# Kernel optimization log

Measured on AMD Instinct MI355X. Metric: run time of the kernel, lower is better.

Reference implementation:

```python
import jax, jax.numpy as jnp
import numpy as np

B, L = 32, 4096
OBS_DIM, ACT_DIM = 32, 8
D_MODEL, D_STATE, N_LAYERS = 64, 16, 2
EXPAND, D_CONV = 2, 4
D_INNER = EXPAND * D_MODEL          # 128
DT_RANK = -(-D_MODEL // 16)         # ceil(64/16) = 4


def _layer_norm(x, w, b, eps=1e-5):
    m = x.mean(-1, keepdims=True)
    v = ((x - m) ** 2).mean(-1, keepdims=True)
    return (x - m) * jax.lax.rsqrt(v + eps) * w + b


def _mamba_block(x, in_proj_W, conv_w, conv_b, x_proj_W, dt_proj_W, dt_proj_b, A_log, D, out_proj_W):
    # x: (B, L, d_model) -> (B, L, d_model)
    xz = jnp.einsum('bld,ed->ble', x, in_proj_W)              # (B, L, 2*d_inner)
    u, z = jnp.split(xz, 2, axis=-1)
    # causal depthwise conv over time (groups = d_inner)
    uc = jax.lax.conv_general_dilated(u.swapaxes(1, 2), conv_w, (1,), [(D_CONV - 1, 0)],
                                      feature_group_count=D_INNER)
    u = jax.nn.silu((uc + conv_b[None, :, None]).swapaxes(1, 2))  # (B, L, d_inner)
    proj = jnp.einsum('bld,ed->ble', u, x_proj_W)             # (B, L, dt_rank + 2*d_state)
    dt = jax.nn.softplus(jnp.einsum('blr,dr->bld', proj[..., :DT_RANK], dt_proj_W) + dt_proj_b)
    Bm = proj[..., DT_RANK:DT_RANK + D_STATE]                 # (B, L, d_state)
    Cm = proj[..., DT_RANK + D_STATE:]                        # (B, L, d_state)
    A = -jnp.exp(A_log)                                       # (d_inner, d_state)

    def step(h, inp):
        u_t, dt_t, B_t, C_t = inp                              # (B,d_inner),(B,d_inner),(B,d_state),(B,d_state)
        h = h * jnp.exp(dt_t[..., None] * A) + (dt_t * u_t)[..., None] * B_t[:, None, :]
        return h, jnp.einsum('bds,bs->bd', h, C_t)

    h0 = jnp.zeros((x.shape[0], D_INNER, D_STATE), x.dtype)
    _, ys = jax.lax.scan(step, h0, (u.swapaxes(0, 1), dt.swapaxes(0, 1),
                                    Bm.swapaxes(0, 1), Cm.swapaxes(0, 1)))
    y = ys.swapaxes(0, 1) + u * D                              # skip term D*u
    y = y * jax.nn.silu(z)                                     # gated output
    return jnp.einsum('bld,od->blo', y, out_proj_W)


def setup_inputs() -> dict:
    key = jax.random.key(0)
    ks = jax.random.split(key, 10)
    s = 0.05
    return {
        'obs': jax.random.normal(ks[0], (B, L, OBS_DIM), jnp.float32),
        'obs_mean': jnp.zeros((OBS_DIM,), jnp.float32),
        'obs_scale': jnp.ones((OBS_DIM,), jnp.float32),
        'ln_in_w': jnp.ones((OBS_DIM,), jnp.float32),
        'ln_in_b': jnp.zeros((OBS_DIM,), jnp.float32),
        'W_in': jax.random.normal(ks[1], (D_MODEL, OBS_DIM), jnp.float32) * s,
        'b_in': jnp.zeros((D_MODEL,), jnp.float32),
        'norm_w': jnp.ones((N_LAYERS, D_MODEL), jnp.float32),
        'norm_b': jnp.zeros((N_LAYERS, D_MODEL), jnp.float32),
        'in_proj_W': jax.random.normal(ks[2], (N_LAYERS, 2 * D_INNER, D_MODEL), jnp.float32) * s,
        'conv_w': jax.random.normal(ks[3], (N_LAYERS, D_INNER, 1, D_CONV), jnp.float32) * s,
        'conv_b': jnp.zeros((N_LAYERS, D_INNER), jnp.float32),
        'x_proj_W': jax.random.normal(ks[4], (N_LAYERS, DT_RANK + 2 * D_STATE, D_INNER), jnp.float32) * s,
        'dt_proj_W': jax.random.normal(ks[5], (N_LAYERS, D_INNER, DT_RANK), jnp.float32) * s,
        'dt_proj_b': jax.random.normal(ks[6], (N_LAYERS, D_INNER), jnp.float32) * s,
        'A_log': jnp.log(jnp.broadcast_to(jnp.arange(1, D_STATE + 1, dtype=jnp.float32), (N_LAYERS, D_INNER, D_STATE))),
        'D': jnp.ones((N_LAYERS, D_INNER), jnp.float32),
        'out_proj_W': jax.random.normal(ks[7], (N_LAYERS, D_MODEL, D_INNER), jnp.float32) * s,
        'W_out': jax.random.normal(ks[8], (ACT_DIM, D_MODEL), jnp.float32) * s,
        'b_out': jnp.zeros((ACT_DIM,), jnp.float32),
    }


def reference(obs, obs_mean, obs_scale, ln_in_w, ln_in_b, W_in, b_in, norm_w, norm_b,
              in_proj_W, conv_w, conv_b, x_proj_W, dt_proj_W, dt_proj_b, A_log, D,
              out_proj_W, W_out, b_out):
    x = (obs - obs_mean) / obs_scale                 # _normalize_observations
    x = _layer_norm(x, ln_in_w, ln_in_b)             # input_norm
    x = jnp.einsum('blo,do->bld', x, W_in) + b_in    # input_layer
    for i in range(N_LAYERS):                        # x = x + block(norm(x))
        x = x + _mamba_block(_layer_norm(x, norm_w[i], norm_b[i]),
                             in_proj_W[i], conv_w[i], conv_b[i], x_proj_W[i],
                             dt_proj_W[i], dt_proj_b[i], A_log[i], D[i], out_proj_W[i])
    return jnp.einsum('bld,ad->bla', x, W_out) + b_out  # output_layer
```

## Files before the change

kernel.cpp:

```cpp
#include <hip/hip_runtime.h>
#include <hip/hip_bf16.h>

#define BB 32
#define LL 4096
#define DI 128
#define DSS 16
#define NLAY 2
#define NC 128
#define CT 32
#define MROWS (BB*LL)

typedef short v8s __attribute__((ext_vector_type(8)));
typedef float v4f __attribute__((ext_vector_type(4)));
#define MFMA16(a,b,c) __builtin_amdgcn_mfma_f32_16x16x32_bf16(a,b,c,0,0,0)

#define B_X     0ull
#define B_UCOOK 16777216ull
#define B_Z     50331648ull
#define B_DTY   83886080ull
#define B_BC    117440512ull
#define B_H     125829120ull
#define B_SDT   142606336ull
#define B_WGT   144703488ull
#define B_PACK  144977920ull

#define WM_OMEAN   0
#define WM_OSCALE  32
#define WM_LNW     64
#define WM_LNB     96
#define WM_WIN     128
#define WM_BIN     2176
#define WM_NORMW   2240
#define WM_NORMB   2368
#define WM_INPROJ  2496
#define WM_CONVW   35264
#define WM_CONVB   36288
#define WM_XPROJ   36544
#define WM_DTW     45760
#define WM_DTB     46784
#define WM_ALOG    47040
#define WM_D       51136
#define WM_OUTPROJ 51392
#define WM_WOUT    67776
#define WM_BOUT    68288

#define PK_WIN 0
#define PK_INP 2048
#define PK_XP  34816
#define PK_OP  47104

__device__ __forceinline__ float ldf(const void* p, long long i, bool bf) {
  if (bf) {
    unsigned int u = ((unsigned int)((const unsigned short*)p)[i]) << 16;
    float f; __builtin_memcpy(&f, &u, 4); return f;
  }
  return ((const float*)p)[i];
}
__device__ __forceinline__ float s2f(short s){
  unsigned int u = ((unsigned int)(unsigned short)s) << 16;
  float f; __builtin_memcpy(&f, &u, 4); return f;
}
__device__ __forceinline__ short f2s(float f){
  unsigned int u; __builtin_memcpy(&u, &f, 4);
  u += 0x7fffu + ((u >> 16) & 1u);
  return (short)(u >> 16);
}
__device__ __forceinline__ float siluf(float x){
  return x * __builtin_amdgcn_rcpf(1.f + __expf(-x));
}
__device__ __forceinline__ float softplusf(float x){
  return fmaxf(x,0.f) + __logf(1.f + __expf(-fabsf(x)));
}
__device__ __forceinline__ void powtree(float e1, float pw[16]){
  pw[0]=e1; pw[1]=e1*e1; pw[3]=pw[1]*pw[1]; pw[7]=pw[3]*pw[3]; pw[15]=pw[7]*pw[7];
  pw[2]=pw[1]*e1; pw[4]=pw[3]*e1; pw[5]=pw[3]*pw[1]; pw[6]=pw[3]*pw[2];
  pw[8]=pw[7]*e1; pw[9]=pw[7]*pw[1]; pw[10]=pw[7]*pw[2]; pw[11]=pw[7]*pw[3];
  pw[12]=pw[7]*pw[4]; pw[13]=pw[7]*pw[5]; pw[14]=pw[7]*pw[6];
}

struct PtrPack { const void* p[19]; };

__global__ __launch_bounds__(256) void k_cvt(PtrPack pp, float* __restrict__ dst,
                                             short* __restrict__ pk) {
  bool bf = ((const unsigned short*)pp.p[14])[1] != 0;
  int b = blockIdx.x;
  if (b < 19) {
    const int SZ[19] = {32,32,32,32,2048,64,128,128,32768,1024,256,9216,1024,256,4096,256,16384,512,8};
    const int OF[19] = {WM_OMEAN,WM_OSCALE,WM_LNW,WM_LNB,WM_WIN,WM_BIN,WM_NORMW,WM_NORMB,
                        WM_INPROJ,WM_CONVW,WM_CONVB,WM_XPROJ,WM_DTW,WM_DTB,WM_ALOG,WM_D,
                        WM_OUTPROJ,WM_WOUT,WM_BOUT};
    const void* src = pp.p[b];
    int n = SZ[b], o = OF[b];
    for (int j = threadIdx.x; j < n; j += 256) dst[o + j] = ldf(src, j, bf);
  } else {
    int pi = b - 19;
    const int SRC[7]  = {4,8,8,11,11,16,16};
    const int LOFF[7] = {0,0,16384,0,4608,0,8192};
    const int NTA[7]  = {4,16,16,3,3,4,4};
    const int KTA[7]  = {1,2,2,4,4,4,4};
    const int KA[7]   = {32,64,64,128,128,128,128};
    const int NRA[7]  = {64,256,256,36,36,64,64};
    const int DOFF[7] = {PK_WIN, PK_INP, PK_INP+16384, PK_XP, PK_XP+6144, PK_OP, PK_OP+8192};
    const void* src = pp.p[SRC[pi]];
    int ktc = KTA[pi], K = KA[pi], nr = NRA[pi], doff = DOFF[pi], loff = LOFF[pi];
    int tot = NTA[pi]*ktc*512;
    for (int i = threadIdx.x; i < tot; i += 256) {
      int j = i & 7, lane = (i >> 3) & 63, t2 = i >> 9;
      int kt = t2 % ktc, ntile = t2 / ktc;
      int n = ntile*16 + (lane & 15);
      int k = kt*32 + (lane >> 4)*8 + j;
      float v = (n < nr) ? ldf(src, loff + (long long)n*K + k, bf) : 0.f;
      pk[doff + i] = f2s(v);
    }
  }
}

__global__ __launch_bounds__(256) void k_input(const void* __restrict__ obs,
    const float* __restrict__ wgt, const void* __restrict__ alog_raw,
    short* __restrict__ x, const short* __restrict__ pk)
{
  __shared__ short lA[64*40];
  bool bf = ((const unsigned short*)alog_raw)[1] != 0;
  int t = threadIdx.x;
  long long row0 = (long long)blockIdx.x * 64;
  {
    int m = t >> 2, q = t & 3;
    const float* om  = wgt + WM_OMEAN + q*8;
    const float* osc = wgt + WM_OSCALE + q*8;
    const float* lw  = wgt + WM_LNW + q*8;
    const float* lb  = wgt + WM_LNB + q*8;
    long long base = (row0 + m)*32 + q*8;
    float v[8]; float s1 = 0.f, s2 = 0.f;
    #pragma unroll
    for (int i = 0; i < 8; ++i) {
      float o = ldf(obs, base + i, bf);
      o = (o - om[i]) / osc[i];
      v[i] = o; s1 += o; s2 += o*o;
    }
    s1 += __shfl_xor(s1,1); s1 += __shfl_xor(s1,2);
    s2 += __shfl_xor(s2,1); s2 += __shfl_xor(s2,2);
    float mean = s1*(1.f/32.f);
    float var  = s2*(1.f/32.f) - mean*mean;
    float rs = rsqrtf(var + 1e-5f);
    #pragma unroll
    for (int i = 0; i < 8; ++i)
      lA[m*40 + q*8 + i] = f2s((v[i]-mean)*rs*lw[i] + lb[i]);
  }
  __syncthreads();
  int w = t >> 6, L = t & 63;
  v8s b = *(const v8s*)(pk + PK_WIN + (w*64 + L)*8);
  v4f zero = {0.f,0.f,0.f,0.f};
  v4f acc[4];
  #pragma unroll
  for (int mt = 0; mt < 4; ++mt) {
    v8s a = *(const v8s*)&lA[(mt*16 + (L&15))*40 + (L>>4)*8];
    acc[mt] = MFMA16(a, b, zero);
  }
  int col = w*16 + (L & 15);
  float bi = wgt[WM_BIN + col];
  #pragma unroll
  for (int mt = 0; mt < 4; ++mt)
    #pragma unroll
    for (int r = 0; r < 4; ++r) {
      int row = mt*16 + (L>>4)*4 + r;
      x[(row0+row)*64 + col] = f2s(acc[mt][r] + bi);
    }
}

__global__ __launch_bounds__(256) void k_fused1(
    const short* __restrict__ x, const float* __restrict__ wgt,
    const short* __restrict__ pk, short* __restrict__ ucook,
    short* __restrict__ z, short* __restrict__ dty,
    short* __restrict__ bcb, short* __restrict__ hbuf,
    float* __restrict__ sdtbuf, int layer)
{
  __shared__ char smem[40752];
  short* lA    = (short*)smem;
  short* lU    = (short*)smem;
  short* lUraw = (short*)(smem + 17408);
  float* lnxh  = (float*)(smem + 35632);
  float* lB    = (float*)(smem + 35632);
  float* lDtr  = (float*)(smem + 39728);
  int t = threadIdx.x;
  long long row0 = (long long)blockIdx.x * 64;
  int l0 = (int)(row0 & (LL-1));

  {
    int m = t >> 2, q = t & 3;
    const v8s* xr = (const v8s*)(x + (row0+m)*64 + q*16);
    v8s x0 = xr[0], x1 = xr[1];
    float v[16]; float s1 = 0.f, s2 = 0.f;
    #pragma unroll
    for (int j = 0; j < 8; ++j) { v[j] = s2f(x0[j]); v[8+j] = s2f(x1[j]); }
    #pragma unroll
    for (int j = 0; j < 16; ++j) { s1 += v[j]; s2 += v[j]*v[j]; }
    s1 += __shfl_xor(s1,1); s1 += __shfl_xor(s1,2);
    s2 += __shfl_xor(s2,1); s2 += __shfl_xor(s2,2);
    float mean = s1*(1.f/64.f);
    float var  = s2*(1.f/64.f) - mean*mean;
    float rs = rsqrtf(var + 1e-5f);
    const float* nw = wgt + WM_NORMW + layer*64 + q*16;
    const float* nb = wgt + WM_NORMB + layer*64 + q*16;
    #pragma unroll
    for (int j = 0; j < 16; ++j)
      lA[m*72 + q*16 + j] = f2s((v[j]-mean)*rs*nw[j] + nb[j]);
  }
  if (l0 > 0 && t < 192) {
    int hr = t >> 6, lane = t & 63;
    float xv = s2f(x[(row0 - 3 + hr)*64 + lane]);
    float s1 = xv, sq = xv*xv;
    #pragma unroll
    for (int o = 1; o < 64; o <<= 1) { s1 += __shfl_xor(s1, o); sq += __shfl_xor(sq, o); }
    float mean = s1*(1.f/64.f);
    float var  = sq*(1.f/64.f) - mean*mean;
    float rs = rsqrtf(var + 1e-5f);
    lnxh[hr*64 + lane] = (xv-mean)*rs*wgt[WM_NORMW + layer*64 + lane]
                       + wgt[WM_NORMB + layer*64 + lane];
  }
  __syncthreads();
  if (l0 > 0) {
    for (int i = t; i < 384; i += 256) {
      int hr = i >> 7, d = i & 127;
      const float* W  = wgt + WM_INPROJ + layer*16384 + d*64;
      const float* ln = lnxh + hr*64;
      float acc = 0.f;
      #pragma unroll 8
      for (int k2 = 0; k2 < 64; ++k2) acc = fmaf(ln[k2], W[k2], acc);
      lUraw[hr*136 + d] = f2s(acc);
    }
  } else {
    for (int i = t; i < 384; i += 256) lUraw[(i>>7)*136 + (i&127)] = 0;
  }
  {
    int w = t >> 6, L = t & 63;
    v8s af[4][2];
    #pragma unroll
    for (int mt = 0; mt < 4; ++mt)
      #pragma unroll
      for (int kt = 0; kt < 2; ++kt)
        af[mt][kt] = *(const v8s*)&lA[(mt*16 + (L&15))*72 + kt*32 + (L>>4)*8];
    v4f zero = {0.f,0.f,0.f,0.f};
    v4f acc[4][4];
    #pragma unroll
    for (int mt = 0; mt < 4; ++mt)
      #pragma unroll
      for (int nt = 0; nt < 4; ++nt) acc[mt][nt] = zero;
    const short* pb = pk + PK_INP + layer*16384;
    #pragma unroll
    for (int nt = 0; nt < 4; ++nt)
      #pragma unroll
      for (int kt = 0; kt < 2; ++kt) {
        v8s b = *(const v8s*)(pb + (((w*4+nt)*2 + kt)*64 + L)*8);
        #pragma unroll
        for (int mt = 0; mt < 4; ++mt)
          acc[mt][nt] = MFMA16(af[mt][kt], b, acc[mt][nt]);
      }
    #pragma unroll
    for (int nt = 0; nt < 4; ++nt) {
      int col = w*64 + nt*16 + (L & 15);
      #pragma unroll
      for (int mt = 0; mt < 4; ++mt)
        #pragma unroll
        for (int r = 0; r < 4; ++r) {
          int row = mt*16 + (L>>4)*4 + r;
          float val = acc[mt][nt][r];
          if (col < 128) lUraw[(row+3)*136 + col] = f2s(val);
          else           z[(row0+row)*DI + col-128] = f2s(val);
        }
    }
  }
  __syncthreads();
  {
    int k = t & 127, half = t >> 7, r0c = half*32;
    const float* CW = wgt + WM_CONVW + layer*512 + k*4;
    float cw0=CW[0], cw1=CW[1], cw2=CW[2], cw3=CW[3];
    float cb = wgt[WM_CONVB + layer*128 + k];
    float q0 = s2f(lUraw[(r0c+0)*136 + k]);
    float q1 = s2f(lUraw[(r0c+1)*136 + k]);
    float q2 = s2f(lUraw[(r0c+2)*136 + k]);
    #pragma unroll 4
    for (int j = 0; j < 32; ++j) {
      float q3 = s2f(lUraw[(r0c+j+3)*136 + k]);
      float cv = cb + cw0*q0 + cw1*q1 + cw2*q2 + cw3*q3;
      q0=q1; q1=q2; q2=q3;
      short cs = f2s(siluf(cv));
      lU[(r0c+j)*136 + k] = cs;
      ucook[(row0+r0c+j)*DI + k] = cs;
    }
  }
  __syncthreads();
  {
    int w = t >> 6, L = t & 63;
    v8s a[4];
    #pragma unroll
    for (int kt = 0; kt < 4; ++kt)
      a[kt] = *(const v8s*)&lU[(w*16 + (L&15))*136 + kt*32 + (L>>4)*8];
    v4f zero = {0.f,0.f,0.f,0.f};
    v4f acc[3] = {zero, zero, zero};
    const short* pb = pk + PK_XP + layer*6144;
    #pragma unroll
    for (int nt = 0; nt < 3; ++nt)
      #pragma unroll
      for (int kt = 0; kt < 4; ++kt) {
        v8s b = *(const v8s*)(pb + ((nt*4 + kt)*64 + L)*8);
        acc[nt] = MFMA16(a[kt], b, acc[nt]);
      }
    int colL = L & 15, qd = L >> 4;
    #pragma unroll
    for (int nt = 0; nt < 3; ++nt) {
      int col = nt*16 + colL;
      #pragma unroll
      for (int r = 0; r < 4; ++r) {
        int row = w*16 + qd*4 + r;
        float val = acc[nt][r];
        if (col < 4) lDtr[row*4 + col] = val;
        else if (col < 36) {
          bcb[(row0+row)*32 + col-4] = f2s(val);
          if (col < 20) lB[row*16 + col-4] = val;
        }
      }
    }
  }
  __syncthreads();
  {
    int d = t & 127, c2 = t >> 7;
    int r0s = c2*32;
    const float* AL = wgt + WM_ALOG + layer*2048 + d*16;
    float a0 = -__expf(AL[0]);
    float eps[16];
    #pragma unroll
    for (int s = 0; s < 16; ++s) eps[s] = -__expf(AL[s]) - (float)(s+1)*a0;
    const float* DWp = wgt + WM_DTW + layer*512 + d*4;
    float dw0=DWp[0], dw1=DWp[1], dw2=DWp[2], dw3=DWp[3];
    float db = wgt[WM_DTB + layer*128 + d];
    float h[16] = {};
    float sdt = 0.f;
    for (int m = 0; m < CT; ++m) {
      float4 p = *(const float4*)&lDtr[(r0s+m)*4];
      float dtv = softplusf(db + p.x*dw0 + p.y*dw1 + p.z*dw2 + p.w*dw3);
      dty[(row0+r0s+m)*DI + d] = f2s(dtv);
      float u = s2f(lU[(r0s+m)*136 + d]);
      float dtu = dtv*u; sdt += dtv;
      float e1 = __expf(dtv*a0);
      float pw[16]; powtree(e1, pw);
      float Bf[16];
      const float4* B4 = (const float4*)(lB + (r0s+m)*16);
      *(float4*)&Bf[0] = B4[0]; *(float4*)&Bf[4] = B4[1];
      *(float4*)&Bf[8] = B4[2]; *(float4*)&Bf[12] = B4[3];
      #pragma unroll
      for (int s = 0; s < 16; ++s) {
        float xx = dtv*eps[s];
        float dec = fmaf(xx, pw[s], pw[s]);
        h[s] = fmaf(h[s], dec, dtu*Bf[s]);
      }
    }
    int b = blockIdx.x >> 6;
    int c = ((blockIdx.x & 63) << 1) + c2;
    long long cidx = (long long)b*NC + c;
    #pragma unroll
    for (int s = 0; s < 16; ++s)
      hbuf[(cidx*16 + s)*DI + d] = f2s(h[s]);
    sdtbuf[cidx*DI + d] = sdt;
  }
}

__global__ __launch_bounds__(256) void k_scan2(
    short* __restrict__ hbuf, const float* __restrict__ sdtbuf,
    const float* __restrict__ wgt, int layer)
{
  int idx = blockIdx.x*256 + threadIdx.x;
  int d = idx & (DI-1);
  int s = (idx >> 7) & 15;
  int b = idx >> 11;
  float a = -__expf(wgt[WM_ALOG + layer*2048 + d*16 + s]);
  float h = 0.f;
  for (int c = 0; c < NC; ++c) {
    long long i2 = ((long long)(b*NC + c)*16 + s)*DI + d;
    float hl = s2f(hbuf[i2]);
    hbuf[i2] = f2s(h);
    float E = __expf(a * sdtbuf[(long long)(b*NC + c)*DI + d]);
    h = hl + h*E;
  }
}

__global__ __launch_bounds__(256) void k_fused3(
    const short* __restrict__ ucook, const short* __restrict__ dty,
    const short* __restrict__ bcb, const short* __restrict__ zb,
    const short* __restrict__ hbuf, const float* __restrict__ wgt,
    const short* __restrict__ pk, short* __restrict__ x,
    const void* __restrict__ alog_raw, void* __restrict__ out,
    int layer, int do_wout)
{
  __shared__ short lY[64*136];
  __shared__ float lBC[64*32];
  int t = threadIdx.x;
  long long row0 = (long long)blockIdx.x * 64;
  for (int i = t; i < 64*32; i += 256) lBC[i] = s2f(bcb[row0*32 + i]);
  __syncthreads();
  {
    int d = t & 127, c2 = t >> 7;
    int r0s = c2*32;
    const float* AL = wgt + WM_ALOG + layer*2048 + d*16;
    float a0 = -__expf(AL[0]);
    float eps[16];
    #pragma unroll
    for (int s = 0; s < 16; ++s) eps[s] = -__expf(AL[s]) - (float)(s+1)*a0;
    float Dd = wgt[WM_D + layer*128 + d];
    int b = blockIdx.x >> 6;
    int c = ((blockIdx.x & 63) << 1) + c2;
    long long cidx = (long long)b*NC + c;
    float h[16];
    #pragma unroll
    for (int s = 0; s < 16; ++s) h[s] = s2f(hbuf[(cidx*16 + s)*DI + d]);
    for (int m = 0; m < CT; ++m) {
      long long row = row0 + r0s + m;
      float dtv = s2f(dty[row*DI + d]);
      float u   = s2f(ucook[row*DI + d]);
      float zv  = s2f(zb[row*DI + d]);
      float dtu = dtv*u;
      float e1 = __expf(dtv*a0);
      float pw[16]; powtree(e1, pw);
      float BCf[32];
      const float4* BC4 = (const float4*)(lBC + (r0s+m)*32);
      #pragma unroll
      for (int q4 = 0; q4 < 8; ++q4) *(float4*)&BCf[q4*4] = BC4[q4];
      float y = 0.f;
      #pragma unroll
      for (int s = 0; s < 16; ++s) {
        float xx = dtv*eps[s];
        float dec = fmaf(xx, pw[s], pw[s]);
        h[s] = fmaf(h[s], dec, dtu*BCf[s]);
        y = fmaf(h[s], BCf[16+s], y);
      }
      lY[(r0s+m)*136 + d] = f2s((y + u*Dd)*siluf(zv));
    }
  }
  __syncthreads();
  float xnew[4][4];
  int w = t >> 6, L = t & 63;
  {
    v4f zero = {0.f,0.f,0.f,0.f};
    v4f acc[4] = {zero, zero, zero, zero};
    const short* pb = pk + PK_OP + layer*8192;
    #pragma unroll
    for (int kt = 0; kt < 4; ++kt) {
      v8s b = *(const v8s*)(pb + ((w*4 + kt)*64 + L)*8);
      #pragma unroll
      for (int mt = 0; mt < 4; ++mt) {
        v8s a = *(const v8s*)&lY[(mt*16 + (L&15))*136 + kt*32 + (L>>4)*8];
        acc[mt] = MFMA16(a, b, acc[mt]);
      }
    }
    int col = w*16 + (L & 15);
    #pragma unroll
    for (int mt = 0; mt < 4; ++mt)
      #pragma unroll
      for (int r = 0; r < 4; ++r) {
        int row = mt*16 + (L>>4)*4 + r;
        long long g = (row0+row)*64 + col;
        xnew[mt][r] = s2f(x[g]) + acc[mt][r];
        if (!do_wout) x[g] = f2s(xnew[mt][r]);
      }
  }
  if (do_wout) {
    __syncthreads();
    int col = w*16 + (L & 15);
    #pragma unroll
    for (int mt = 0; mt < 4; ++mt)
      #pragma unroll
      for (int r = 0; r < 4; ++r) {
        int row = mt*16 + (L>>4)*4 + r;
        lY[row*72 + col] = f2s(xnew[mt][r]);
      }
    __syncthreads();
    bool bf = ((const unsigned short*)alog_raw)[1] != 0;
    for (int i = t; i < 512; i += 256) {
      int m = i >> 3, aa = i & 7;
      const float* W = wgt + WM_WOUT + aa*64;
      const short* xr = &lY[m*72];
      float acc = wgt[WM_BOUT + aa];
      #pragma unroll
      for (int j8 = 0; j8 < 8; ++j8) {
        v8s xv = *(const v8s*)&xr[j8*8];
        #pragma unroll
        for (int j = 0; j < 8; ++j) acc = fmaf(s2f(xv[j]), W[j8*8+j], acc);
      }
      long long oi = (row0 + m)*8 + aa;
      if (bf) ((__hip_bfloat16*)out)[oi] = __float2bfloat16(acc);
      else    ((float*)out)[oi] = acc;
    }
  }
}

extern "C" void kernel_launch(void* const* d_in, const int* in_sizes, int n_in,
                              void* d_out, int out_size, void* d_ws, size_t ws_size,
                              hipStream_t stream)
{
  char* wsb = (char*)d_ws;
  short* x     = (short*)(wsb + B_X);
  short* ucook = (short*)(wsb + B_UCOOK);
  short* zb    = (short*)(wsb + B_Z);
  short* dty   = (short*)(wsb + B_DTY);
  short* bcb   = (short*)(wsb + B_BC);
  short* hbuf  = (short*)(wsb + B_H);
  float* sdt   = (float*)(wsb + B_SDT);
  float* wgt   = (float*)(wsb + B_WGT);
  short* pk    = (short*)(wsb + B_PACK);

  PtrPack pp;
  for (int i = 0; i < 19; ++i) pp.p[i] = d_in[i+1];
  const void* obs  = d_in[0];
  const void* alog = d_in[15];

  k_cvt  <<<dim3(26),        dim3(256), 0, stream>>>(pp, wgt, pk);
  k_input<<<dim3(MROWS/64),  dim3(256), 0, stream>>>(obs, wgt, alog, x, pk);
  for (int layer = 0; layer < NLAY; ++layer) {
    k_fused1<<<dim3(MROWS/64),      dim3(256), 0, stream>>>(x, wgt, pk, ucook, zb, dty, bcb, hbuf, sdt, layer);
    k_scan2 <<<dim3(BB*DSS*DI/256), dim3(256), 0, stream>>>(hbuf, sdt, wgt, layer);
    k_fused3<<<dim3(MROWS/64),      dim3(256), 0, stream>>>(ucook, dty, bcb, zb, hbuf, wgt, pk, x,
                                                            alog, d_out, layer, layer == NLAY-1);
  }
}
```

Measured before the change: 482.1 us.

## Fuse input projection into first layer, transpose chunk-state layout, prefetch scan inputs

Folds the input normalization and input-layer matmul into the layer-0 fused1 kernel. This removes one launch and the global round trip of x, with the halo rows recomputed from obs. It also transposes the hbuf and sdtbuf layouts so each scan2 thread reads its chunk sequence contiguously with vector loads, instead of making strided scalar accesses. fused3 software-prefetches the next timestep's dt/u/z values. The cost is redundant halo computation, plus scattered stores in fused1 and fused3 under the new layout.

```diff
diff --git a/kernel.cpp b/kernel.cpp
--- a/kernel.cpp
+++ b/kernel.cpp
@@ -115,83 +115,119 @@
   }
 }
 
-__global__ __launch_bounds__(256) void k_input(const void* __restrict__ obs,
-    const float* __restrict__ wgt, const void* __restrict__ alog_raw,
-    short* __restrict__ x, const short* __restrict__ pk)
+__global__ __launch_bounds__(256) void k_fused1(
+    const void* __restrict__ obs, short* __restrict__ x,
+    const float* __restrict__ wgt, const short* __restrict__ pk,
+    short* __restrict__ ucook, short* __restrict__ z,
+    short* __restrict__ dty, short* __restrict__ bcb,
+    short* __restrict__ hbuf, float* __restrict__ sdtbuf,
+    const void* __restrict__ alog_raw, int layer)
 {
-  __shared__ short lA[64*40];
-  bool bf = ((const unsigned short*)alog_raw)[1] != 0;
-  int t = threadIdx.x;
-  long long row0 = (long long)blockIdx.x * 64;
-  {
-    int m = t >> 2, q = t & 3;
-    const float* om  = wgt + WM_OMEAN + q*8;
-    const float* osc = wgt + WM_OSCALE + q*8;
-    const float* lw  = wgt + WM_LNW + q*8;
-    const float* lb  = wgt + WM_LNB + q*8;
-    long long base = (row0 + m)*32 + q*8;
-    float v[8]; float s1 = 0.f, s2 = 0.f;
-    #pragma unroll
-    for (int i = 0; i < 8; ++i) {
-      float o = ldf(obs, base + i, bf);
-      o = (o - om[i]) / osc[i];
-      v[i] = o; s1 += o; s2 += o*o;
-    }
-    s1 += __shfl_xor(s1,1); s1 += __shfl_xor(s1,2);
-    s2 += __shfl_xor(s2,1); s2 += __shfl_xor(s2,2);
-    float mean = s1*(1.f/32.f);
-    float var  = s2*(1.f/32.f) - mean*mean;
-    float rs = rsqrtf(var + 1e-5f);
-    #pragma unroll
-    for (int i = 0; i < 8; ++i)
-      lA[m*40 + q*8 + i] = f2s((v[i]-mean)*rs*lw[i] + lb[i]);
-  }
-  __syncthreads();
-  int w = t >> 6, L = t & 63;
-  v8s b = *(const v8s*)(pk + PK_WIN + (w*64 + L)*8);
-  v4f zero = {0.f,0.f,0.f,0.f};
-  v4f acc[4];
-  #pragma unroll
-  for (int mt = 0; mt < 4; ++mt) {
-    v8s a = *(const v8s*)&lA[(mt*16 + (L&15))*40 + (L>>4)*8];
-    acc[mt] = MFMA16(a, b, zero);
-  }
-  int col = w*16 + (L & 15);
-  float bi = wgt[WM_BIN + col];
-  #pragma unroll
-  for (int mt = 0; mt < 4; ++mt)
-    #pragma unroll
-    for (int r = 0; r < 4; ++r) {
-      int row = mt*16 + (L>>4)*4 + r;
-      x[(row0+row)*64 + col] = f2s(acc[mt][r] + bi);
-    }
-}
-
-__global__ __launch_bounds__(256) void k_fused1(
-    const short* __restrict__ x, const float* __restrict__ wgt,
-    const short* __restrict__ pk, short* __restrict__ ucook,
-    short* __restrict__ z, short* __restrict__ dty,
-    short* __restrict__ bcb, short* __restrict__ hbuf,
-    float* __restrict__ sdtbuf, int layer)
-{
-  __shared__ char smem[40752];
+  __shared__ char smem[35632];
   short* lA    = (short*)smem;
   short* lU    = (short*)smem;
+  float* lnxh  = (float*)(smem + 16384);
   short* lUraw = (short*)(smem + 17408);
-  float* lnxh  = (float*)(smem + 35632);
-  float* lB    = (float*)(smem + 35632);
-  float* lDtr  = (float*)(smem + 39728);
+  float* lB    = (float*)(smem + 17408);
+  float* lDtr  = (float*)(smem + 21504);
+  short* lOb   = (short*)(smem + 17408);
+  float* lObsH = (float*)(smem + 25600);
   int t = threadIdx.x;
   long long row0 = (long long)blockIdx.x * 64;
   int l0 = (int)(row0 & (LL-1));
 
+  if (layer == 0) {
+    bool bf = ((const unsigned short*)alog_raw)[1] != 0;
+    {
+      int m = t >> 2, q = t & 3;
+      const float* om  = wgt + WM_OMEAN + q*8;
+      const float* osc = wgt + WM_OSCALE + q*8;
+      const float* lw  = wgt + WM_LNW + q*8;
+      const float* lb  = wgt + WM_LNB + q*8;
+      long long base = (row0 + m)*32 + q*8;
+      float v[8]; float s1 = 0.f, s2 = 0.f;
+      #pragma unroll
+      for (int i = 0; i < 8; ++i) {
+        float o = ldf(obs, base + i, bf);
+        o = (o - om[i]) / osc[i];
+        v[i] = o; s1 += o; s2 += o*o;
+      }
+      s1 += __shfl_xor(s1,1); s1 += __shfl_xor(s1,2);
+      s2 += __shfl_xor(s2,1); s2 += __shfl_xor(s2,2);
+      float mean = s1*(1.f/32.f);
+      float var  = s2*(1.f/32.f) - mean*mean;
+      float rs = rsqrtf(var + 1e-5f);
+      #pragma unroll
+      for (int i = 0; i < 8; ++i)
+        lOb[m*40 + q*8 + i] = f2s((v[i]-mean)*rs*lw[i] + lb[i]);
+    }
+    if (l0 > 0 && t < 96) {
+      int hr = t >> 5, i = t & 31;
+      long long base = (row0 - 3 + hr)*32;
+      float s1 = 0.f, s2 = 0.f, vi = 0.f;
+      for (int j = 0; j < 32; ++j) {
+        float o = (ldf(obs, base + j, bf) - wgt[WM_OMEAN+j]) / wgt[WM_OSCALE+j];
+        if (j == i) vi = o;
+        s1 += o; s2 += o*o;
+      }
+      float mean = s1*(1.f/32.f);
+      float var  = s2*(1.f/32.f) - mean*mean;
+      float rs = rsqrtf(var + 1e-5f);
+      lObsH[hr*32 + i] = (vi-mean)*rs*wgt[WM_LNW+i] + wgt[WM_LNB+i];
+    }
+    __syncthreads();
+    v4f xacc[4];
+    {
+      int w = t >> 6, L = t & 63;
+      v8s b = *(const v8s*)(pk + PK_WIN + (w*64 + L)*8);
+      v4f zero = {0.f,0.f,0.f,0.f};
+      #pragma unroll
+      for (int mt = 0; mt < 4; ++mt) {
+        v8s a = *(const v8s*)&lOb[(mt*16 + (L&15))*40 + (L>>4)*8];
+        xacc[mt] = MFMA16(a, b, zero);
+      }
+    }
+    if (l0 > 0 && t < 192) {
+      int hr = t >> 6, cc = t & 63;
+      const float* W  = wgt + WM_WIN + cc*32;
+      const float* ob = lObsH + hr*32;
+      float acc = wgt[WM_BIN + cc];
+      #pragma unroll 8
+      for (int i = 0; i < 32; ++i) acc = fmaf(ob[i], W[i], acc);
+      lnxh[hr*64 + cc] = acc;
+    }
+    __syncthreads();
+    {
+      int w = t >> 6, L = t & 63;
+      int col = w*16 + (L & 15);
+      float bi = wgt[WM_BIN + col];
+      #pragma unroll
+      for (int mt = 0; mt < 4; ++mt)
+        #pragma unroll
+        for (int r = 0; r < 4; ++r) {
+          int row = mt*16 + (L>>4)*4 + r;
+          short s = f2s(xacc[mt][r] + bi);
+          lA[row*72 + col] = s;
+          x[(row0+row)*64 + col] = s;
+        }
+    }
+    __syncthreads();
+  }
+
   {
     int m = t >> 2, q = t & 3;
-    const v8s* xr = (const v8s*)(x + (row0+m)*64 + q*16);
-    v8s x0 = xr[0], x1 = xr[1];
     float v[16]; float s1 = 0.f, s2 = 0.f;
-    #pragma unroll
-    for (int j = 0; j < 8; ++j) { v[j] = s2f(x0[j]); v[8+j] = s2f(x1[j]); }
+    if (layer == 0) {
+      v8s x0 = *(const v8s*)&lA[m*72 + q*16];
+      v8s x1 = *(const v8s*)&lA[m*72 + q*16 + 8];
+      #pragma unroll
+      for (int j = 0; j < 8; ++j) { v[j] = s2f(x0[j]); v[8+j] = s2f(x1[j]); }
+    } else {
+      const v8s* xr = (const v8s*)(x + (row0+m)*64 + q*16);
+      v8s x0 = xr[0], x1 = xr[1];
+      #pragma unroll
+      for (int j = 0; j < 8; ++j) { v[j] = s2f(x0[j]); v[8+j] = s2f(x1[j]); }
+    }
     #pragma unroll
     for (int j = 0; j < 16; ++j) { s1 += v[j]; s2 += v[j]*v[j]; }
     s1 += __shfl_xor(s1,1); s1 += __shfl_xor(s1,2);
@@ -207,7 +243,8 @@
   }
   if (l0 > 0 && t < 192) {
     int hr = t >> 6, lane = t & 63;
-    float xv = s2f(x[(row0 - 3 + hr)*64 + lane]);
+    float xv = (layer == 0) ? lnxh[hr*64 + lane]
+                            : s2f(x[(row0 - 3 + hr)*64 + lane]);
     float s1 = xv, sq = xv*xv;
     #pragma unroll
     for (int o = 1; o < 64; o <<= 1) { s1 += __shfl_xor(s1, o); sq += __shfl_xor(sq, o); }
@@ -356,11 +393,10 @@
     }
     int b = blockIdx.x >> 6;
     int c = ((blockIdx.x & 63) << 1) + c2;
-    long long cidx = (long long)b*NC + c;
     #pragma unroll
     for (int s = 0; s < 16; ++s)
-      hbuf[(cidx*16 + s)*DI + d] = f2s(h[s]);
-    sdtbuf[cidx*DI + d] = sdt;
+      hbuf[((long long)((b*16 + s)*128 + d))*NC + c] = f2s(h[s]);
+    sdtbuf[((long long)(b*128 + d))*NC + c] = sdt;
   }
 }
 
@@ -369,17 +405,25 @@
     const float* __restrict__ wgt, int layer)
 {
   int idx = blockIdx.x*256 + threadIdx.x;
-  int d = idx & (DI-1);
-  int s = (idx >> 7) & 15;
-  int b = idx >> 11;
+  int d = idx & 127, s = (idx >> 7) & 15, b = idx >> 11;
   float a = -__expf(wgt[WM_ALOG + layer*2048 + d*16 + s]);
+  long long bh = (long long)idx * NC;
+  long long bs = ((long long)(b*128 + d)) * NC;
   float h = 0.f;
-  for (int c = 0; c < NC; ++c) {
-    long long i2 = ((long long)(b*NC + c)*16 + s)*DI + d;
-    float hl = s2f(hbuf[i2]);
-    hbuf[i2] = f2s(h);
-    float E = __expf(a * sdtbuf[(long long)(b*NC + c)*DI + d]);
-    h = hl + h*E;
+  for (int c8 = 0; c8 < NC/8; ++c8) {
+    v8s hl8 = *(const v8s*)(hbuf + bh + c8*8);
+    float4 sa = *(const float4*)(sdtbuf + bs + c8*8);
+    float4 sb = *(const float4*)(sdtbuf + bs + c8*8 + 4);
+    float sd[8] = {sa.x,sa.y,sa.z,sa.w,sb.x,sb.y,sb.z,sb.w};
+    union { v8s v; short o[8]; } outp;
+    #pragma unroll
+    for (int j = 0; j < 8; ++j) {
+      float hl = s2f(hl8[j]);
+      float E = __expf(a * sd[j]);
+      outp.o[j] = f2s(h);
+      h = fmaf(h, E, hl);
+    }
+    *(v8s*)(hbuf + bh + c8*8) = outp.v;
   }
 }
 
@@ -408,15 +452,19 @@
     float Dd = wgt[WM_D + layer*128 + d];
     int b = blockIdx.x >> 6;
     int c = ((blockIdx.x & 63) << 1) + c2;
-    long long cidx = (long long)b*NC + c;
     float h[16];
     #pragma unroll
-    for (int s = 0; s < 16; ++s) h[s] = s2f(hbuf[(cidx*16 + s)*DI + d]);
+    for (int s = 0; s < 16; ++s)
+      h[s] = s2f(hbuf[((long long)((b*16 + s)*128 + d))*NC + c]);
+    long long rb = (row0 + r0s)*DI + d;
+    short pdt = dty[rb], pu = ucook[rb], pz = zb[rb];
     for (int m = 0; m < CT; ++m) {
-      long long row = row0 + r0s + m;
-      float dtv = s2f(dty[row*DI + d]);
-      float u   = s2f(ucook[row*DI + d]);
-      float zv  = s2f(zb[row*DI + d]);
+      short ndt = 0, nu = 0, nz = 0;
+      if (m < CT-1) {
+        long long rn = rb + (long long)(m+1)*DI;
+        ndt = dty[rn]; nu = ucook[rn]; nz = zb[rn];
+      }
+      float dtv = s2f(pdt), u = s2f(pu), zv = s2f(pz);
       float dtu = dtv*u;
       float e1 = __expf(dtv*a0);
       float pw[16]; powtree(e1, pw);
@@ -433,6 +481,7 @@
         y = fmaf(h[s], BCf[16+s], y);
       }
       lY[(r0s+m)*136 + d] = f2s((y + u*Dd)*siluf(zv));
+      pdt = ndt; pu = nu; pz = nz;
     }
   }
   __syncthreads();
@@ -512,10 +561,10 @@
   const void* obs  = d_in[0];
   const void* alog = d_in[15];
 
-  k_cvt  <<<dim3(26),        dim3(256), 0, stream>>>(pp, wgt, pk);
-  k_input<<<dim3(MROWS/64),  dim3(256), 0, stream>>>(obs, wgt, alog, x, pk);
+  k_cvt<<<dim3(26), dim3(256), 0, stream>>>(pp, wgt, pk);
   for (int layer = 0; layer < NLAY; ++layer) {
-    k_fused1<<<dim3(MROWS/64),      dim3(256), 0, stream>>>(x, wgt, pk, ucook, zb, dty, bcb, hbuf, sdt, layer);
+    k_fused1<<<dim3(MROWS/64),      dim3(256), 0, stream>>>(obs, x, wgt, pk, ucook, zb, dty, bcb,
+                                                            hbuf, sdt, alog, layer);
     k_scan2 <<<dim3(BB*DSS*DI/256), dim3(256), 0, stream>>>(hbuf, sdt, wgt, layer);
     k_fused3<<<dim3(MROWS/64),      dim3(256), 0, stream>>>(ucook, dty, bcb, zb, hbuf, wgt, pk, x,
                                                             alog, d_out, layer, layer == NLAY-1);
```

After: 594.4 us. +23.3%, slower.
